# Performance work log

Measured on AMD Instinct MI355X. Metric: run time of the kernel, lower is better.

Reference implementation:

```python
import jax, jax.numpy as jnp
import numpy as np

N_NODES = 50000
HIDDEN = 256
DEPTH = 6
NUM_GRAPHS = 500


def _build_graph(n):
    # 4-regular directed graph: node i -> (i+1, i-1, i+5, i-5) mod n.
    offs = np.array([1, -1, 5, -5], dtype=np.int64)
    src = np.repeat(np.arange(n, dtype=np.int64), 4)
    dst = (src + np.tile(offs, n)) % n
    # incoming edge ids of node u (edge id = 4*src + offset_index)
    u = np.arange(n, dtype=np.int64)
    incoming = np.stack([4 * ((u - 1) % n) + 0,
                         4 * ((u + 1) % n) + 1,
                         4 * ((u - 5) % n) + 2,
                         4 * ((u + 5) % n) + 3], axis=1)  # [n,4]
    E = 4 * n
    pred = incoming[src]           # [E,4] candidate line-graph predecessors of edge e
    pred_src = pred // 4           # source node of each predecessor edge
    keep = pred_src != dst[:, None]  # drop backtracking edge (exactly 1 per row)
    lg_src = pred[keep]                                   # [3E]
    lg_dst = np.repeat(np.arange(E, dtype=np.int64), 4)[keep.ravel()]  # [3E]
    return src, dst, lg_src, lg_dst


def setup_inputs() -> dict:
    key = jax.random.key(0)
    ks = jax.random.split(key, 8)
    n, H = N_NODES, HIDDEN
    E = 4 * n
    _, dst, lg_src, lg_dst = _build_graph(n)
    graph_ids = np.arange(n, dtype=np.int64) // (n // NUM_GRAPHS)
    s = 0.02  # small weight scale keeps relu message passing stable over DEPTH iters
    return {
        "x_nodes": jax.random.normal(ks[0], (n, 35), jnp.float32),
        "x_edges": jax.random.normal(ks[1], (E, 40), jnp.float32),
        "t_m": jax.random.normal(ks[2], (E, H), jnp.float32) * 0.1,
        "W_i": jax.random.normal(ks[3], (40, H), jnp.float32) * s,
        "W_h": jax.random.normal(ks[4], (H, H), jnp.float32) * s,
        "W_o": jax.random.normal(ks[5], (35 + H, H), jnp.float32) * s,
        "b_o": jax.random.normal(ks[6], (H,), jnp.float32) * s,
        "edge_dst": jnp.asarray(dst, jnp.int32),
        "lg_src": jnp.asarray(lg_src, jnp.int32),
        "lg_dst": jnp.asarray(lg_dst, jnp.int32),
        "graph_ids": jnp.asarray(graph_ids, jnp.int32),
        "num_graphs": NUM_GRAPHS,
    }


def reference(x_nodes, x_edges, t_m, W_i, W_h, W_o, b_o,
              edge_dst, lg_src, lg_dst, graph_ids, num_graphs):
    E = x_edges.shape[0]
    n = x_nodes.shape[0]
    binput = x_edges @ W_i                       # W_i has no bias
    g_m = jax.nn.relu(binput)                    # [E,H] per-edge message
    # tree-message aggregation over line graph is constant across depth iters
    t_agg = jax.ops.segment_sum(t_m[lg_src], lg_dst, num_segments=E)
    for _ in range(DEPTH - 1):
        g_agg = jax.ops.segment_sum(g_m[lg_src], lg_dst, num_segments=E)
        g_m = jax.nn.relu(binput + (g_agg + t_agg) @ W_h)
    # edge -> dst-node aggregation (copy_e + sum)
    nei1 = jax.ops.segment_sum(g_m, edge_dst, num_segments=n)
    nei2 = jax.ops.segment_sum(t_m, edge_dst, num_segments=n)
    ainput = jnp.concatenate([x_nodes, nei1 + nei2], axis=1)  # [n, 35+H]
    atom_hiddens = jax.nn.relu(ainput @ W_o + b_o)
    # dgl.mean_nodes: per-graph mean of node features
    sums = jax.ops.segment_sum(atom_hiddens, graph_ids, num_segments=num_graphs)
    counts = jax.ops.segment_sum(jnp.ones((n, 1), atom_hiddens.dtype), graph_ids,
                                 num_segments=num_graphs)
    return sums / counts
```

## Files before the change

### kernel.cpp

```cpp
#include <hip/hip_runtime.h>


#define H 256

typedef __attribute__((ext_vector_type(4))) float f32x4;
typedef __attribute__((ext_vector_type(8))) short bf16x8;

#define MFMA(a, b, c) __builtin_amdgcn_mfma_f32_16x16x32_bf16((a), (b), (c), 0, 0, 0)

__device__ __forceinline__ float bf2f(ushort u) {
  union { unsigned int i; float f; } v; v.i = ((unsigned int)u) << 16; return v.f;
}
__device__ __forceinline__ ushort f2bf(float f) {
  union { float f; unsigned int i; } v; v.f = f;
  unsigned int i = v.i;
  i += 0x7fffu + ((i >> 16) & 1u);
  return (ushort)(i >> 16);
}

union AFrag { bf16x8 v; ushort u[8]; };

__device__ __forceinline__ int edge_delta(int o) {
  return ((o & 2) ? 5 : 1) * ((o & 1) ? -1 : 1);
}

__device__ __forceinline__ int phi(int L) {
  return (L & ~31) | (((L >> 2) & 1) << 4) | (((L >> 3) & 3) << 2) | (L & 3);
}

__global__ __launch_bounds__(256) void prep_weights_kernel(
    const float* __restrict__ Wh, const float* __restrict__ Wi, const float* __restrict__ Wo,
    ushort* __restrict__ WhF, ushort* __restrict__ WiTF,
    ushort* __restrict__ WoT1, ushort* __restrict__ WoT2) {
  const int nn = blockIdx.x;
  const int t = threadIdx.x;
  const int w = phi(nn);
  const int nfg = w >> 4, l15w = w & 15;
  const int ks = t >> 5, kg = (t >> 3) & 3, i = t & 7;
  WhF[((nfg * 8 + ks) << 9) + ((kg << 4) + l15w) * 8 + i] = f2bf(Wh[t * H + nn]);
  WoT2[nn * H + t] = f2bf(Wo[(35 + t) * H + nn]);
  if (t < 64) {
    WiTF[((nfg * 2 + ks) << 9) + ((kg << 4) + l15w) * 8 + i] =
        (t < 40) ? f2bf(Wi[t * H + nn]) : (ushort)0;
    WoT1[nn * 64 + t] = (t < 35) ? f2bf(Wo[t * H + nn]) : (ushort)0;
  }
}

__global__ __launch_bounds__(256) void sum_tm_kernel(
    const float* __restrict__ t_m, ushort* __restrict__ t3, ushort* __restrict__ t4,
    int n, int useT4) {
  const int idx = blockIdx.x * 256 + threadIdx.x;
  const int s = idx >> 5;
  if (s >= n) return;
  const int cg = (idx & 31) * 8;
  int im1 = s - 1; if (im1 < 0) im1 += n;
  int ip1 = s + 1; if (ip1 >= n) ip1 -= n;
  int im5 = s - 5; if (im5 < 0) im5 += n;
  int ip5 = s + 5; if (ip5 >= n) ip5 -= n;
  const size_t e0 = (size_t)(4 * im1 + 0) * H + cg;
  const size_t e1 = (size_t)(4 * ip1 + 1) * H + cg;
  const size_t e2 = (size_t)(4 * im5 + 2) * H + cg;
  const size_t e3 = (size_t)(4 * ip5 + 3) * H + cg;
  f32x4 v0a = *(const f32x4*)(t_m + e0), v0b = *(const f32x4*)(t_m + e0 + 4);
  f32x4 v1a = *(const f32x4*)(t_m + e1), v1b = *(const f32x4*)(t_m + e1 + 4);
  f32x4 v2a = *(const f32x4*)(t_m + e2), v2b = *(const f32x4*)(t_m + e2 + 4);
  f32x4 v3a = *(const f32x4*)(t_m + e3), v3b = *(const f32x4*)(t_m + e3 + 4);
  f32x4 Sa = v0a + v1a + v2a + v3a;
  f32x4 Sb = v0b + v1b + v2b + v3b;
  f32x4 ra[4] = {Sa - v1a, Sa - v0a, Sa - v3a, Sa - v2a};
  f32x4 rb[4] = {Sb - v1b, Sb - v0b, Sb - v3b, Sb - v2b};
  const int cgs = cg >> 5;
  const int cgk = (cg >> 3) & 3;
#pragma unroll
  for (int o = 0; o < 4; ++o) {
    AFrag a;
#pragma unroll
    for (int i = 0; i < 4; ++i) { a.u[i] = f2bf(ra[o][i]); a.u[4 + i] = f2bf(rb[o][i]); }
    const int e = 4 * s + o;
    *(bf16x8*)(t3 + (((size_t)(e >> 4)) << 12) + (cgs << 9) + (((cgk << 4) + (e & 15)) << 3)) = a.v;
  }
  if (useT4) {
    AFrag a;
#pragma unroll
    for (int i = 0; i < 4; ++i) { a.u[i] = f2bf(Sa[i]); a.u[4 + i] = f2bf(Sb[i]); }
    *(bf16x8*)(t4 + (size_t)s * H + cg) = a.v;
  }
}

__global__ __launch_bounds__(1024, 8) void prologue_kernel(
    const float* __restrict__ x_edges, const ushort* __restrict__ t3,
    const ushort* __restrict__ WhF, const ushort* __restrict__ WiTF,
    ushort* __restrict__ tb, ushort* __restrict__ g0, int E, int n) {
  extern __shared__ ushort lds[];
  const int tid = threadIdx.x;
  const int wid = tid >> 6, lane = tid & 63, l15 = lane & 15, kg = lane >> 4;
  const int ch = blockIdx.x & 1;

  {
    const bf16x8* src = (const bf16x8*)(WhF) + ch * 4096;
    bf16x8* dstl = (bf16x8*)lds;
#pragma unroll
    for (int j = 0; j < 4; ++j) dstl[tid + j * 1024] = src[tid + j * 1024];
  }
  __syncthreads();

  const int row0 = ((blockIdx.x >> 1) << 8) + wid * 16;
  if (row0 >= E) return;
  const int r = row0 + l15;
  const size_t blkoff = ((size_t)(row0 >> 4)) << 12;

  const float* xp = x_edges + (size_t)r * 40;
  f32x4 xa0 = *(const f32x4*)(xp + kg * 8);
  f32x4 xa1 = *(const f32x4*)(xp + kg * 8 + 4);
  f32x4 xb0, xb1;
  if (kg == 0) { xb0 = *(const f32x4*)(xp + 32); xb1 = *(const f32x4*)(xp + 36); }

  const ushort* t3r = t3 + blkoff + lane * 8;
  bf16x8 av0 = *(const bf16x8*)(t3r);
  bf16x8 av1 = *(const bf16x8*)(t3r + 512);

  f32x4 acc[8];
#pragma unroll
  for (int i = 0; i < 8; ++i) acc[i] = (f32x4){0.f, 0.f, 0.f, 0.f};

  AFrag bx0, bx1;
#pragma unroll
  for (int i = 0; i < 4; ++i) { bx0.u[i] = f2bf(xa0[i]); bx0.u[4 + i] = f2bf(xa1[i]); }
  if (kg == 0) {
#pragma unroll
    for (int i = 0; i < 4; ++i) { bx1.u[i] = f2bf(xb0[i]); bx1.u[4 + i] = f2bf(xb1[i]); }
  } else {
#pragma unroll
    for (int i = 0; i < 8; ++i) bx1.u[i] = 0;
  }
#pragma unroll
  for (int nf = 0; nf < 8; ++nf) {
    bf16x8 a0 = *(const bf16x8*)(WiTF + (((ch * 8 + nf) * 2 + 0) << 9) + lane * 8);
    acc[nf] = MFMA(a0, bx0.v, acc[nf]);
    bf16x8 a1 = *(const bf16x8*)(WiTF + (((ch * 8 + nf) * 2 + 1) << 9) + lane * 8);
    acc[nf] = MFMA(a1, bx1.v, acc[nf]);
  }

  ushort* gout = g0 + blkoff + ((size_t)(ch * 4) << 9) + lane * 8;
#pragma unroll
  for (int tt = 0; tt < 4; ++tt) {
    AFrag pk;
#pragma unroll
    for (int i = 0; i < 4; ++i) {
      pk.u[i]     = f2bf(fmaxf(acc[2 * tt][i], 0.f));
      pk.u[4 + i] = f2bf(fmaxf(acc[2 * tt + 1][i], 0.f));
    }
    *(bf16x8*)(gout + (tt << 9)) = pk.v;
  }

#pragma unroll
  for (int ks = 0; ks < 8; ++ks) {
    bf16x8 av2;
    if (ks < 6) av2 = *(const bf16x8*)(t3r + (ks + 2) * 512);
#pragma unroll
    for (int nf = 0; nf < 8; ++nf) {
      bf16x8 a = *(const bf16x8*)(lds + ((nf * 8 + ks) << 9) + (lane << 3));
      acc[nf] = MFMA(a, av0, acc[nf]);
    }
    av0 = av1; av1 = av2;
  }

  ushort* tbp = tb + blkoff + ((size_t)(ch * 4) << 9) + lane * 8;
#pragma unroll
  for (int tt = 0; tt < 4; ++tt) {
    AFrag pk;
#pragma unroll
    for (int i = 0; i < 4; ++i) {
      pk.u[i]     = f2bf(acc[2 * tt][i]);
      pk.u[4 + i] = f2bf(acc[2 * tt + 1][i]);
    }
    *(bf16x8*)(tbp + (tt << 9)) = pk.v;
  }
}

__global__ __launch_bounds__(1024, 8) void mp_iter_kernel(
    const ushort* __restrict__ gOld, const ushort* __restrict__ tb,
    const ushort* __restrict__ WhF, ushort* __restrict__ gNew, int E, int n) {
  extern __shared__ ushort lds[];
  const int tid = threadIdx.x;
  const int wid = tid >> 6, lane = tid & 63, l15 = lane & 15, kg = lane >> 4;
  const int ch = blockIdx.x & 1;

  {
    const bf16x8* src = (const bf16x8*)(WhF) + ch * 4096;
    bf16x8* dstl = (bf16x8*)lds;
#pragma unroll
    for (int j = 0; j < 4; ++j) dstl[tid + j * 1024] = src[tid + j * 1024];
  }
  __syncthreads();

  const int row0 = ((blockIdx.x >> 1) << 8) + wid * 16;
  if (row0 >= E) return;
  const int r = row0 + l15;
  const size_t blkoff = ((size_t)(row0 >> 4)) << 12;

  const int s = r >> 2, o = r & 3;
  int sm = s - edge_delta(o);
  if (sm < 0) sm += n; else if (sm >= n) sm -= n;
  const int lam = 4 * sm + o;
  const ushort* gr = gOld + (((size_t)(lam >> 4)) << 12) + (((kg << 4) + (lam & 15)) << 3);

  bf16x8 av0 = *(const bf16x8*)(gr);
  bf16x8 av1 = *(const bf16x8*)(gr + 512);

  f32x4 acc[8];
#pragma unroll
  for (int i = 0; i < 8; ++i) acc[i] = (f32x4){0.f, 0.f, 0.f, 0.f};

#pragma unroll
  for (int ks = 0; ks < 8; ++ks) {
    bf16x8 av2;
    if (ks < 6) av2 = *(const bf16x8*)(gr + (ks + 2) * 512);
#pragma unroll
    for (int nf = 0; nf < 8; ++nf) {
      bf16x8 a = *(const bf16x8*)(lds + ((nf * 8 + ks) << 9) + (lane << 3));
      acc[nf] = MFMA(a, av0, acc[nf]);
    }
    av0 = av1; av1 = av2;
  }

  bf16x8 tbv[4];
  const ushort* tbp = tb + blkoff + ((size_t)(ch * 4) << 9) + lane * 8;
#pragma unroll
  for (int tt = 0; tt < 4; ++tt) tbv[tt] = *(const bf16x8*)(tbp + (tt << 9));

  ushort* gout = gNew + blkoff + ((size_t)(ch * 4) << 9) + lane * 8;
#pragma unroll
  for (int tt = 0; tt < 4; ++tt) {
    AFrag pk;
#pragma unroll
    for (int i = 0; i < 4; ++i) {
      const float G0 = acc[2 * tt][i];
      const float G1 = acc[2 * tt + 1][i];
      const float t0 = G0 + __shfl_xor(G0, 2);
      const float S0 = t0 + __shfl_xor(t0, 1);
      const float t1 = G1 + __shfl_xor(G1, 2);
      const float S1 = t1 + __shfl_xor(t1, 1);
      const float d0 = __shfl_xor(G0, 1);
      const float d1 = __shfl_xor(G1, 1);
      const float v0 = bf2f((ushort)tbv[tt][i])     + (S0 - d0);
      const float v1 = bf2f((ushort)tbv[tt][4 + i]) + (S1 - d1);
      pk.u[i]     = f2bf(fmaxf(v0, 0.f));
      pk.u[4 + i] = f2bf(fmaxf(v1, 0.f));
    }
    *(bf16x8*)(gout + (tt << 9)) = pk.v;
  }
}

__global__ __launch_bounds__(256) void readout_kernel(
    const float* __restrict__ x_nodes, const float* __restrict__ t_m,
    const ushort* __restrict__ gP, const ushort* __restrict__ t4,
    const float* __restrict__ b_o,
    const ushort* __restrict__ WoT1, const ushort* __restrict__ WoT2,
    float* __restrict__ out, int n, int npg, int useT4) {
  const int gidx = blockIdx.x;
  const int wid = threadIdx.x >> 6;
  const int lane = threadIdx.x & 63;
  const int l15 = lane & 15;
  const int kg = lane >> 4;
  const int u0 = gidx * npg;

  __shared__ float red[H];

  f32x4 acc[2][16];
#pragma unroll
  for (int m = 0; m < 2; ++m)
#pragma unroll
    for (int i = 0; i < 16; ++i) acc[m][i] = (f32x4){0.f, 0.f, 0.f, 0.f};

  int uu[2]; bool mv[2]; int inc[2][4];
#pragma unroll
  for (int m = 0; m < 2; ++m) {
    const int mf = wid * 2 + m;
    const int rl = mf * 16 + l15;
    mv[m] = rl < npg;
    const int u = u0 + rl;
    uu[m] = u;
    if (mv[m]) {
      inc[m][0] = 4 * ((u - 1 + n) % n);
      inc[m][1] = 4 * ((u + 1) % n) + 1;
      inc[m][2] = 4 * ((u - 5 + n) % n) + 2;
      inc[m][3] = 4 * ((u + 5) % n) + 3;
    } else {
      inc[m][0] = inc[m][1] = inc[m][2] = inc[m][3] = 0;
    }
  }

#pragma unroll
  for (int ks = 0; ks < 2; ++ks) {
    const int k = ks * 32 + kg * 8;
#pragma unroll
    for (int m = 0; m < 2; ++m) {
      AFrag a;
#pragma unroll
      for (int i = 0; i < 8; ++i) {
        const int kk = k + i;
        a.u[i] = (mv[m] && kk < 35) ? f2bf(x_nodes[(size_t)uu[m] * 35 + kk]) : (ushort)0;
      }
#pragma unroll
      for (int nf = 0; nf < 16; ++nf) {
        bf16x8 b = *(const bf16x8*)(WoT1 + (nf * 16 + l15) * 64 + k);
        acc[m][nf] = MFMA(a.v, b, acc[m][nf]);
      }
    }
  }

#pragma unroll
  for (int ks = 0; ks < 8; ++ks) {
    const int k = ks * 32 + kg * 8;
#pragma unroll
    for (int m = 0; m < 2; ++m) {
      AFrag a;
      if (mv[m]) {
        float s[8];
#pragma unroll
        for (int i = 0; i < 8; ++i) s[i] = 0.f;
#pragma unroll
        for (int j = 0; j < 4; ++j) {
          const int e = inc[m][j];
          const ushort* gp = gP + (((size_t)(e >> 4)) << 12) + ((size_t)ks << 9)
                           + (((kg << 4) + (e & 15)) << 3);
          bf16x8 gv = *(const bf16x8*)gp;
#pragma unroll
          for (int i = 0; i < 8; ++i) s[i] += bf2f((ushort)gv[i]);
        }
        if (useT4) {
          bf16x8 tv = *(const bf16x8*)(t4 + (size_t)uu[m] * H + k);
#pragma unroll
          for (int i = 0; i < 8; ++i) s[i] += bf2f((ushort)tv[i]);
        } else {
#pragma unroll
          for (int j = 0; j < 4; ++j) {
            const float* tp = t_m + (size_t)inc[m][j] * H + k;
            f32x4 t0 = *(const f32x4*)tp;
            f32x4 t1 = *(const f32x4*)(tp + 4);
#pragma unroll
            for (int i = 0; i < 4; ++i) { s[i] += t0[i]; s[4 + i] += t1[i]; }
          }
        }
#pragma unroll
        for (int i = 0; i < 8; ++i) a.u[i] = f2bf(s[i]);
      } else {
#pragma unroll
        for (int i = 0; i < 8; ++i) a.u[i] = 0;
      }
#pragma unroll
      for (int nf = 0; nf < 16; ++nf) {
        bf16x8 b = *(const bf16x8*)(WoT2 + (nf * 16 + l15) * H + k);
        acc[m][nf] = MFMA(a.v, b, acc[m][nf]);
      }
    }
  }

  red[threadIdx.x] = 0.f;
  __syncthreads();

#pragma unroll
  for (int nf = 0; nf < 16; ++nf) {
    const int col = nf * 16 + l15;
    const float bias = b_o[col];
    float cs = 0.f;
#pragma unroll
    for (int m = 0; m < 2; ++m) {
#pragma unroll
      for (int j = 0; j < 4; ++j) {
        const int rr = (wid * 2 + m) * 16 + kg * 4 + j;
        if (rr < npg) cs += fmaxf(acc[m][nf][j] + bias, 0.f);
      }
    }
    cs += __shfl_xor(cs, 16);
    cs += __shfl_xor(cs, 32);
    if (kg == 0) atomicAdd(&red[col], cs);
  }
  __syncthreads();
  out[(size_t)gidx * H + threadIdx.x] = red[threadIdx.x] * (1.0f / (float)npg);
}

extern "C" void kernel_launch(void* const* d_in, const int* in_sizes, int n_in,
                              void* d_out, int out_size, void* d_ws, size_t ws_size,
                              hipStream_t stream) {
  const float* x_nodes = (const float*)d_in[0];
  const float* x_edges = (const float*)d_in[1];
  const float* t_m     = (const float*)d_in[2];
  const float* W_i     = (const float*)d_in[3];
  const float* W_h     = (const float*)d_in[4];
  const float* W_o     = (const float*)d_in[5];
  const float* b_o     = (const float*)d_in[6];
  (void)n_in;

  const int n = in_sizes[0] / 35;
  const int E = in_sizes[1] / 40;
  const int num_graphs = out_size / H;
  const int npg = n / num_graphs;

  char* ws = (char*)d_ws;
  ushort* WhF  = (ushort*)(ws);
  ushort* WiTF = (ushort*)(ws + 131072);
  ushort* WoT1 = (ushort*)(ws + 164 * 1024);
  ushort* WoT2 = (ushort*)(ws + 200 * 1024);
  size_t off = 336 * 1024;
  const size_t gbytes = (size_t)E * H * 2;
  ushort* tb = (ushort*)(ws + off); off += gbytes;
  ushort* gA = (ushort*)(ws + off); off += gbytes;
  ushort* gB = (ushort*)(ws + off); off += gbytes;
  ushort* t3 = gB;
  const size_t t4bytes = (size_t)n * H * 2;
  const int useT4 = (ws_size >= off + t4bytes) ? 1 : 0;
  ushort* t4 = (ushort*)(ws + off);

  const int nch = (E + 255) >> 8;

  prep_weights_kernel<<<256, 256, 0, stream>>>(W_h, W_i, W_o, WhF, WiTF, WoT1, WoT2);
  sum_tm_kernel<<<(n * 32 + 255) / 256, 256, 0, stream>>>(t_m, t3, t4, n, useT4);
  prologue_kernel<<<2 * nch, 1024, 65536, stream>>>(x_edges, t3, WhF, WiTF, tb, gA, E, n);

  ushort* src = gA;
  ushort* dst = gB;
  for (int it = 0; it < 5; ++it) {
    mp_iter_kernel<<<2 * nch, 1024, 65536, stream>>>(src, tb, WhF, dst, E, n);
    ushort* tmp = src; src = dst; dst = tmp;
  }

  readout_kernel<<<num_graphs, 256, 0, stream>>>(x_nodes, t_m, src, t4, b_o, WoT1, WoT2,
                                                 (float*)d_out, n, npg, useT4);
}
```

Before: 719.9 us.

## Split readout across multiple blocks per graph with global atomics and tiled t4

The readout kernel now assigns one 16-row tile per wave and launches several blocks per graph, so more CUs work on the final stage. Partial per-graph sums are accumulated with global atomicAdd into an output that is zeroed with a memset beforehand. The t4 buffer is also stored in the same tiled fragment layout as the edge messages. This adds a memset launch and global atomic traffic, and makes the float summation order nondeterministic.

Result: slower. 752.6 us (+4.6%).

```diff
diff --git a/kernel.cpp b/kernel.cpp
--- a/kernel.cpp
+++ b/kernel.cpp
@@ -83,7 +83,7 @@
     AFrag a;
 #pragma unroll
     for (int i = 0; i < 4; ++i) { a.u[i] = f2bf(Sa[i]); a.u[4 + i] = f2bf(Sb[i]); }
-    *(bf16x8*)(t4 + (size_t)s * H + cg) = a.v;
+    *(bf16x8*)(t4 + (((size_t)(s >> 4)) << 12) + (cgs << 9) + (((cgk << 4) + (s & 15)) << 3)) = a.v;
   }
 }
 
@@ -252,133 +252,113 @@
   }
 }
 
-__global__ __launch_bounds__(256) void readout_kernel(
+__global__ __launch_bounds__(256, 3) void readout_kernel(
     const float* __restrict__ x_nodes, const float* __restrict__ t_m,
     const ushort* __restrict__ gP, const ushort* __restrict__ t4,
     const float* __restrict__ b_o,
     const ushort* __restrict__ WoT1, const ushort* __restrict__ WoT2,
-    float* __restrict__ out, int n, int npg, int useT4) {
-  const int gidx = blockIdx.x;
+    float* __restrict__ out, int n, int npg, int useT4, int bpg) {
+  const int gidx = blockIdx.x / bpg;
+  const int sub  = blockIdx.x - gidx * bpg;
   const int wid = threadIdx.x >> 6;
   const int lane = threadIdx.x & 63;
   const int l15 = lane & 15;
   const int kg = lane >> 4;
+  const int mf = sub * 4 + wid;
+  const int rl0 = mf * 16;
+  if (rl0 >= npg) return;
   const int u0 = gidx * npg;
-
-  __shared__ float red[H];
-
-  f32x4 acc[2][16];
-#pragma unroll
-  for (int m = 0; m < 2; ++m)
-#pragma unroll
-    for (int i = 0; i < 16; ++i) acc[m][i] = (f32x4){0.f, 0.f, 0.f, 0.f};
-
-  int uu[2]; bool mv[2]; int inc[2][4];
-#pragma unroll
-  for (int m = 0; m < 2; ++m) {
-    const int mf = wid * 2 + m;
-    const int rl = mf * 16 + l15;
-    mv[m] = rl < npg;
-    const int u = u0 + rl;
-    uu[m] = u;
-    if (mv[m]) {
-      inc[m][0] = 4 * ((u - 1 + n) % n);
-      inc[m][1] = 4 * ((u + 1) % n) + 1;
-      inc[m][2] = 4 * ((u - 5 + n) % n) + 2;
-      inc[m][3] = 4 * ((u + 5) % n) + 3;
-    } else {
-      inc[m][0] = inc[m][1] = inc[m][2] = inc[m][3] = 0;
-    }
-  }
+  const int rl = rl0 + l15;
+  const bool mv = rl < npg;
+  const int u = u0 + (mv ? rl : 0);
+
+  int inc[4];
+  inc[0] = 4 * ((u - 1 + n) % n);
+  inc[1] = 4 * ((u + 1) % n) + 1;
+  inc[2] = 4 * ((u - 5 + n) % n) + 2;
+  inc[3] = 4 * ((u + 5) % n) + 3;
+
+  f32x4 acc[16];
+#pragma unroll
+  for (int i = 0; i < 16; ++i) acc[i] = (f32x4){0.f, 0.f, 0.f, 0.f};
 
 #pragma unroll
   for (int ks = 0; ks < 2; ++ks) {
     const int k = ks * 32 + kg * 8;
-#pragma unroll
-    for (int m = 0; m < 2; ++m) {
-      AFrag a;
-#pragma unroll
-      for (int i = 0; i < 8; ++i) {
-        const int kk = k + i;
-        a.u[i] = (mv[m] && kk < 35) ? f2bf(x_nodes[(size_t)uu[m] * 35 + kk]) : (ushort)0;
-      }
-#pragma unroll
-      for (int nf = 0; nf < 16; ++nf) {
-        bf16x8 b = *(const bf16x8*)(WoT1 + (nf * 16 + l15) * 64 + k);
-        acc[m][nf] = MFMA(a.v, b, acc[m][nf]);
-      }
+    AFrag a;
+#pragma unroll
+    for (int i = 0; i < 8; ++i) {
+      const int kk = k + i;
+      a.u[i] = (mv && kk < 35) ? f2bf(x_nodes[(size_t)u * 35 + kk]) : (ushort)0;
+    }
+#pragma unroll
+    for (int nf = 0; nf < 16; ++nf) {
+      bf16x8 b = *(const bf16x8*)(WoT1 + (nf * 16 + l15) * 64 + k);
+      acc[nf] = MFMA(a.v, b, acc[nf]);
     }
   }
 
 #pragma unroll
   for (int ks = 0; ks < 8; ++ks) {
     const int k = ks * 32 + kg * 8;
-#pragma unroll
-    for (int m = 0; m < 2; ++m) {
-      AFrag a;
-      if (mv[m]) {
-        float s[8];
-#pragma unroll
-        for (int i = 0; i < 8; ++i) s[i] = 0.f;
+    AFrag a;
+    if (mv) {
+      float s[8];
+#pragma unroll
+      for (int i = 0; i < 8; ++i) s[i] = 0.f;
+#pragma unroll
+      for (int j = 0; j < 4; ++j) {
+        const int e = inc[j];
+        const ushort* gp = gP + (((size_t)(e >> 4)) << 12) + ((size_t)ks << 9)
+                         + (((kg << 4) + (e & 15)) << 3);
+        bf16x8 gv = *(const bf16x8*)gp;
+#pragma unroll
+        for (int i = 0; i < 8; ++i) s[i] += bf2f((ushort)gv[i]);
+      }
+      if (useT4) {
+        const ushort* tp4 = t4 + (((size_t)(u >> 4)) << 12) + ((size_t)ks << 9)
+                          + (((kg << 4) + (u & 15)) << 3);
+        bf16x8 tv = *(const bf16x8*)tp4;
+#pragma unroll
+        for (int i = 0; i < 8; ++i) s[i] += bf2f((ushort)tv[i]);
+      } else {
 #pragma unroll
         for (int j = 0; j < 4; ++j) {
-          const int e = inc[m][j];
-          const ushort* gp = gP + (((size_t)(e >> 4)) << 12) + ((size_t)ks << 9)
-                           + (((kg << 4) + (e & 15)) << 3);
-          bf16x8 gv = *(const bf16x8*)gp;
-#pragma unroll
-          for (int i = 0; i < 8; ++i) s[i] += bf2f((ushort)gv[i]);
+          const float* tp = t_m + (size_t)inc[j] * H + k;
+          f32x4 t0 = *(const f32x4*)tp;
+          f32x4 t1 = *(const f32x4*)(tp + 4);
+#pragma unroll
+          for (int i = 0; i < 4; ++i) { s[i] += t0[i]; s[4 + i] += t1[i]; }
         }
-        if (useT4) {
-          bf16x8 tv = *(const bf16x8*)(t4 + (size_t)uu[m] * H + k);
-#pragma unroll
-          for (int i = 0; i < 8; ++i) s[i] += bf2f((ushort)tv[i]);
-        } else {
-#pragma unroll
-          for (int j = 0; j < 4; ++j) {
-            const float* tp = t_m + (size_t)inc[m][j] * H + k;
-            f32x4 t0 = *(const f32x4*)tp;
-            f32x4 t1 = *(const f32x4*)(tp + 4);
-#pragma unroll
-            for (int i = 0; i < 4; ++i) { s[i] += t0[i]; s[4 + i] += t1[i]; }
-          }
-        }
-#pragma unroll
-        for (int i = 0; i < 8; ++i) a.u[i] = f2bf(s[i]);
-      } else {
-#pragma unroll
-        for (int i = 0; i < 8; ++i) a.u[i] = 0;
       }
 #pragma unroll
-      for (int nf = 0; nf < 16; ++nf) {
-        bf16x8 b = *(const bf16x8*)(WoT2 + (nf * 16 + l15) * H + k);
-        acc[m][nf] = MFMA(a.v, b, acc[m][nf]);
-      }
-    }
-  }
-
-  red[threadIdx.x] = 0.f;
-  __syncthreads();
-
+      for (int i = 0; i < 8; ++i) a.u[i] = f2bf(s[i]);
+    } else {
+#pragma unroll
+      for (int i = 0; i < 8; ++i) a.u[i] = 0;
+    }
+#pragma unroll
+    for (int nf = 0; nf < 16; ++nf) {
+      bf16x8 b = *(const bf16x8*)(WoT2 + (nf * 16 + l15) * H + k);
+      acc[nf] = MFMA(a.v, b, acc[nf]);
+    }
+  }
+
+  const float inv = 1.0f / (float)npg;
 #pragma unroll
   for (int nf = 0; nf < 16; ++nf) {
     const int col = nf * 16 + l15;
     const float bias = b_o[col];
     float cs = 0.f;
 #pragma unroll
-    for (int m = 0; m < 2; ++m) {
-#pragma unroll
-      for (int j = 0; j < 4; ++j) {
-        const int rr = (wid * 2 + m) * 16 + kg * 4 + j;
-        if (rr < npg) cs += fmaxf(acc[m][nf][j] + bias, 0.f);
-      }
+    for (int j = 0; j < 4; ++j) {
+      const int rr = rl0 + kg * 4 + j;
+      if (rr < npg) cs += fmaxf(acc[nf][j] + bias, 0.f);
     }
     cs += __shfl_xor(cs, 16);
     cs += __shfl_xor(cs, 32);
-    if (kg == 0) atomicAdd(&red[col], cs);
-  }
-  __syncthreads();
-  out[(size_t)gidx * H + threadIdx.x] = red[threadIdx.x] * (1.0f / (float)npg);
+    if (kg == 0) atomicAdd(&out[(size_t)gidx * H + col], cs * inv);
+  }
 }
 
 extern "C" void kernel_launch(void* const* d_in, const int* in_sizes, int n_in,
@@ -414,6 +394,7 @@
   ushort* t4 = (ushort*)(ws + off);
 
   const int nch = (E + 255) >> 8;
+  const int bpg = (npg + 63) / 64;
 
   prep_weights_kernel<<<256, 256, 0, stream>>>(W_h, W_i, W_o, WhF, WiTF, WoT1, WoT2);
   sum_tm_kernel<<<(n * 32 + 255) / 256, 256, 0, stream>>>(t_m, t3, t4, n, useT4);
@@ -426,6 +407,8 @@
     ushort* tmp = src; src = dst; dst = tmp;
   }
 
-  readout_kernel<<<num_graphs, 256, 0, stream>>>(x_nodes, t_m, src, t4, b_o, WoT1, WoT2,
-                                                 (float*)d_out, n, npg, useT4);
-}
+  hipMemsetAsync(d_out, 0, (size_t)out_size * sizeof(float), stream);
+  readout_kernel<<<num_graphs * bpg, 256, 0, stream>>>(x_nodes, t_m, src, t4, b_o,
+                                                       WoT1, WoT2, (float*)d_out,
+                                                       n, npg, useT4, bpg);
+}
```
